# Kernel tuning notes

Hardware: AMD Instinct MI355X
Metric: run time of the kernel (lower is better)

The kernel has to match this reference:

```python
import jax, jax.numpy as jnp
import numpy as np

DIM = 1024
HEADS = 16
HEAD_DIM = DIM // HEADS
EPS = 1e-5


def layer_norm(x, w, b):
    # normalize over last dim (head_dim)
    mu = jnp.mean(x, axis=-1, keepdims=True)
    var = jnp.mean(jnp.square(x - mu), axis=-1, keepdims=True)
    return (x - mu) * jax.lax.rsqrt(var + EPS) * w + b


def setup_inputs() -> dict:
    key = jax.random.key(0)
    ks = jax.random.split(key, 8)
    B, N = 2, 2048
    x = jax.random.normal(ks[0], (B, N, DIM), dtype=jnp.float32)
    mask = jax.random.randint(ks[1], (B, 1, N, N), 0, 2) == 1  # True = masked out
    qkv_w = jax.random.normal(ks[2], (3 * DIM, DIM), dtype=jnp.float32) * (DIM ** -0.5)
    q_norm_w = jnp.ones((HEAD_DIM,), dtype=jnp.float32)
    q_norm_b = jnp.zeros((HEAD_DIM,), dtype=jnp.float32)
    k_norm_w = jnp.ones((HEAD_DIM,), dtype=jnp.float32)
    k_norm_b = jnp.zeros((HEAD_DIM,), dtype=jnp.float32)
    proj_w = jax.random.normal(ks[3], (DIM, DIM), dtype=jnp.float32) * (DIM ** -0.5)
    proj_b = jnp.zeros((DIM,), dtype=jnp.float32)
    return {"x": x, "mask": mask, "qkv_w": qkv_w,
            "q_norm_w": q_norm_w, "q_norm_b": q_norm_b,
            "k_norm_w": k_norm_w, "k_norm_b": k_norm_b,
            "proj_w": proj_w, "proj_b": proj_b}


def reference(x, mask, qkv_w, q_norm_w, q_norm_b, k_norm_w, k_norm_b, proj_w, proj_b):
    B, N, C = x.shape
    H, D = HEADS, HEAD_DIM
    scale = D ** -0.5
    # qkv projection (no bias), split into q,k,v of shape (B,H,N,D)
    qkv = (x @ qkv_w.T).reshape(B, N, 3, H, D).transpose(2, 0, 3, 1, 4)
    q, k, v = qkv[0], qkv[1], qkv[2]
    q = layer_norm(q, q_norm_w, q_norm_b)
    k = layer_norm(k, k_norm_w, k_norm_b)
    q = q * scale
    attn = jnp.einsum("bhnd,bhmd->bhnm", q, k)  # (B,H,N,N)
    attn = jnp.where(mask, -jnp.inf, attn)
    attn = jax.nn.softmax(attn, axis=-1)
    out = jnp.einsum("bhnm,bhmd->bhnd", attn, v)
    out = out.transpose(0, 2, 1, 3).reshape(B, N, C)
    return out @ proj_w.T + proj_b
```

## Files before the change

### kernel.cpp

```cpp
#include <hip/hip_runtime.h>
#include <hip/hip_bf16.h>
#include <math.h>

#define B_    2
#define N_    2048
#define DIM_  1024
#define H_    16
#define HD_   64
#define EPS_  1e-5f
#define SCALE_ 0.125f
#define LOG2E_ 1.4426950408889634f
#define MFIX_  14.0f

typedef __attribute__((ext_vector_type(8))) __bf16 bf16x8;
typedef __attribute__((ext_vector_type(8))) unsigned short ushort8;
typedef __attribute__((ext_vector_type(4))) float f32x4;
typedef __attribute__((ext_vector_type(4))) unsigned int uint4v;

__device__ __forceinline__ unsigned short f2bf(float x) {
    unsigned u = __builtin_bit_cast(unsigned, x);
    u += 0x7fff + ((u >> 16) & 1);
    return (unsigned short)(u >> 16);
}
__device__ __forceinline__ unsigned pk2bf(float a, float b) {
    unsigned ua = __builtin_bit_cast(unsigned, a) + 0x8000u;
    unsigned ub = __builtin_bit_cast(unsigned, b) + 0x8000u;
    return __builtin_amdgcn_perm(ub, ua, 0x07060302);
}

__device__ __forceinline__ void gl_lds16(const void* g, void* l) {
    __builtin_amdgcn_global_load_lds(
        (const __attribute__((address_space(1))) void*)g,
        (__attribute__((address_space(3))) void*)l, 16, 0, 0);
}

__global__ __launch_bounds__(256) void cast_all_bf16(
    const float* __restrict__ x, const float* __restrict__ qkvw,
    const float* __restrict__ pw, unsigned short* __restrict__ out) {
    int i = (blockIdx.x * 256 + threadIdx.x) * 8;
    const float* src;
    if (i < 4194304) src = x + i;
    else if (i < 7340032) src = qkvw + (i - 4194304);
    else src = pw + (i - 7340032);
    float4 v0 = *(const float4*)src;
    float4 v1 = *(const float4*)(src + 4);
    ushort8 r;
    r[0] = f2bf(v0.x); r[1] = f2bf(v0.y); r[2] = f2bf(v0.z); r[3] = f2bf(v0.w);
    r[4] = f2bf(v1.x); r[5] = f2bf(v1.y); r[6] = f2bf(v1.z); r[7] = f2bf(v1.w);
    *(ushort8*)(out + i) = r;
}

__global__ __launch_bounds__(256) void pack_mask(
    const int* __restrict__ mask, unsigned long long* __restrict__ bm) {
    int w = blockIdx.x * 4 + (threadIdx.x >> 6);
    int lane = threadIdx.x & 63;
    int mv = mask[(size_t)w * 64 + lane];
    unsigned long long bits = __ballot(mv != 0);
    if (lane == 0) bm[w] = bits;
}

__global__ __launch_bounds__(256) void gemm_qkv_ln(
    const unsigned short* __restrict__ A, const unsigned short* __restrict__ Bw,
    const float* __restrict__ qnw, const float* __restrict__ qnb,
    const float* __restrict__ knw, const float* __restrict__ knb,
    unsigned short* __restrict__ qbuf, unsigned short* __restrict__ kbuf,
    unsigned short* __restrict__ vbuf) {
    const int K = DIM_;
    __shared__ unsigned short As[128 * 32];
    __shared__ unsigned short Bs[128 * 32];
    const int tid = threadIdx.x;
    const int wave = tid >> 6, lane = tid & 63;
    const int quad = lane >> 4, lcol = lane & 15;
    const int wr = wave >> 1, wc = wave & 1;
    const int row0 = blockIdx.y * 128, col0 = blockIdx.x * 128;

    f32x4 acc[4][4];
#pragma unroll
    for (int i = 0; i < 4; ++i)
#pragma unroll
        for (int j = 0; j < 4; ++j) acc[i][j] = (f32x4){0.f, 0.f, 0.f, 0.f};

    for (int k0 = 0; k0 < K; k0 += 32) {
        __syncthreads();
#pragma unroll
        for (int c = 0; c < 2; ++c) {
            int base = wave * 2048 + c * 1024;
            int myofs = base + lane * 16;
            int r = myofs >> 6;
            int kb = myofs & 63;
            gl_lds16((const char*)A + ((size_t)(row0 + r) * K + k0) * 2 + kb,
                     (char*)As + base);
            gl_lds16((const char*)Bw + ((size_t)(col0 + r) * K + k0) * 2 + kb,
                     (char*)Bs + base);
        }
        __syncthreads();

        bf16x8 af[4], bfr[4];
#pragma unroll
        for (int i = 0; i < 4; ++i) {
            af[i] = *(const bf16x8*)&As[(wr * 64 + i * 16 + lcol) * 32 + quad * 8];
            bfr[i] = *(const bf16x8*)&Bs[(wc * 64 + i * 16 + lcol) * 32 + quad * 8];
        }
#pragma unroll
        for (int i = 0; i < 4; ++i)
#pragma unroll
            for (int j = 0; j < 4; ++j)
                acc[i][j] = __builtin_amdgcn_mfma_f32_16x16x32_bf16(
                    af[i], bfr[j], acc[i][j], 0, 0, 0);
    }

    const int colbase = col0 + wc * 64;
    const int t = colbase >> 10;
    const int h = (colbase & 1023) >> 6;

    if (t < 2) {
        const float* wv = (t == 0) ? qnw : knw;
        const float* bv = (t == 0) ? qnb : knb;
        float wreg[4], breg[4];
#pragma unroll
        for (int j = 0; j < 4; ++j) {
            wreg[j] = wv[j * 16 + lcol];
            breg[j] = bv[j * 16 + lcol];
        }
        const float sc = (t == 0) ? (SCALE_ * LOG2E_) : 1.f;
        unsigned short* obase = (t == 0) ? qbuf : kbuf;
#pragma unroll
        for (int i = 0; i < 4; ++i) {
#pragma unroll
            for (int reg = 0; reg < 4; ++reg) {
                int row = row0 + wr * 64 + i * 16 + quad * 4 + reg;
                int bb = row >> 11, n = row & (N_ - 1);
                float v[4];
#pragma unroll
                for (int j = 0; j < 4; ++j) v[j] = acc[i][j][reg];
                float s = v[0] + v[1] + v[2] + v[3];
                s += __shfl_xor(s, 1);
                s += __shfl_xor(s, 2);
                s += __shfl_xor(s, 4);
                s += __shfl_xor(s, 8);
                float mu = s * (1.f / 64.f);
                float d[4], s2 = 0.f;
#pragma unroll
                for (int j = 0; j < 4; ++j) {
                    d[j] = v[j] - mu;
                    s2 += d[j] * d[j];
                }
                s2 += __shfl_xor(s2, 1);
                s2 += __shfl_xor(s2, 2);
                s2 += __shfl_xor(s2, 4);
                s2 += __shfl_xor(s2, 8);
                float r = rsqrtf(s2 * (1.f / 64.f) + EPS_);
                float o0 = (d[0] * r * wreg[0] + breg[0]) * sc;
                float o1 = (d[1] * r * wreg[1] + breg[1]) * sc;
                float o2 = (d[2] * r * wreg[2] + breg[2]) * sc;
                float o3 = (d[3] * r * wreg[3] + breg[3]) * sc;
                uint2 pk;
                pk.x = pk2bf(o0, o1);
                pk.y = pk2bf(o2, o3);
                *(uint2*)(obase + ((size_t)(bb * H_ + h) * N_ + n) * 64 +
                          lcol * 4) = pk;
            }
        }
    } else {
#pragma unroll
        for (int i = 0; i < 4; ++i) {
#pragma unroll
            for (int reg = 0; reg < 4; ++reg) {
                int row = row0 + wr * 64 + i * 16 + quad * 4 + reg;
                uint2 pk;
                pk.x = pk2bf(acc[i][0][reg], acc[i][1][reg]);
                pk.y = pk2bf(acc[i][2][reg], acc[i][3][reg]);
                *(uint2*)(vbuf + (size_t)row * DIM_ + h * 64 + lcol * 4) = pk;
            }
        }
    }
}

__global__ __launch_bounds__(256) void gemm_proj(
    const unsigned short* __restrict__ A, const unsigned short* __restrict__ Bw,
    const float* __restrict__ bias, float* __restrict__ Cout) {
    const int K = DIM_;
    __shared__ unsigned short As[128 * 32];
    __shared__ unsigned short Bs[64 * 32];
    const int tid = threadIdx.x;
    const int wave = tid >> 6, lane = tid & 63;
    const int quad = lane >> 4, lcol = lane & 15;
    const int row0 = blockIdx.y * 128, col0 = blockIdx.x * 64;

    f32x4 acc[2][4];
#pragma unroll
    for (int i = 0; i < 2; ++i)
#pragma unroll
        for (int j = 0; j < 4; ++j) acc[i][j] = (f32x4){0.f, 0.f, 0.f, 0.f};

    for (int k0 = 0; k0 < K; k0 += 32) {
        __syncthreads();
#pragma unroll
        for (int pi = 0; pi < 3; ++pi) {
            int p = wave * 3 + pi;
            if (p < 8) {
                int base = p * 1024;
                int myofs = base + lane * 16;
                int r = myofs >> 6, kb = myofs & 63;
                gl_lds16((const char*)A + ((size_t)(row0 + r) * K + k0) * 2 + kb,
                         (char*)As + base);
            } else {
                int base = (p - 8) * 1024;
                int myofs = base + lane * 16;
                int r = myofs >> 6, kb = myofs & 63;
                gl_lds16((const char*)Bw + ((size_t)(col0 + r) * K + k0) * 2 + kb,
                         (char*)Bs + base);
            }
        }
        __syncthreads();

        bf16x8 af[2], bfr[4];
#pragma unroll
        for (int i = 0; i < 2; ++i)
            af[i] = *(const bf16x8*)&As[(wave * 32 + i * 16 + lcol) * 32 + quad * 8];
#pragma unroll
        for (int j = 0; j < 4; ++j)
            bfr[j] = *(const bf16x8*)&Bs[(j * 16 + lcol) * 32 + quad * 8];
#pragma unroll
        for (int i = 0; i < 2; ++i)
#pragma unroll
            for (int j = 0; j < 4; ++j)
                acc[i][j] = __builtin_amdgcn_mfma_f32_16x16x32_bf16(
                    af[i], bfr[j], acc[i][j], 0, 0, 0);
    }

#pragma unroll
    for (int i = 0; i < 2; ++i) {
#pragma unroll
        for (int j = 0; j < 4; ++j) {
            int col = col0 + j * 16 + lcol;
            float bv = bias[col];
#pragma unroll
            for (int reg = 0; reg < 4; ++reg) {
                int row = row0 + wave * 32 + i * 16 + quad * 4 + reg;
                Cout[(size_t)row * DIM_ + col] = acc[i][j][reg] + bv;
            }
        }
    }
}

__global__ __launch_bounds__(256) void transpose_v(
    const unsigned short* __restrict__ vbuf, unsigned short* __restrict__ vt) {
    __shared__ unsigned short Ts[64 * 65];
    const int tid = threadIdx.x;
    const int bh = blockIdx.y, n0 = blockIdx.x * 64;
    const int b = bh >> 4, h = bh & 15;
    {
        int r = tid >> 2, s = tid & 3;
        const unsigned short* src =
            vbuf + (size_t)(b * N_ + n0 + r) * DIM_ + h * 64 + s * 16;
#pragma unroll
        for (int i = 0; i < 16; ++i) {
            int p = s * 16 + i;
            int trued = (p >> 2) + (p & 3) * 16;
            Ts[r * 65 + trued] = src[i];
        }
    }
    __syncthreads();
    {
        int d = tid >> 2, kt = tid & 3;
        unsigned short* dstrow = vt + (size_t)(bh * 64 + d) * N_ + n0;
        int P = kt >> 1, t = kt & 1;
#pragma unroll
        for (int q = 0; q < 4; ++q) {
            __align__(8) unsigned short tmp4[4];
#pragma unroll
            for (int j = 0; j < 4; ++j)
                tmp4[j] = Ts[(kt * 16 + q * 4 + j) * 65 + d];
            *(uint2*)(dstrow + P * 32 + q * 8 + t * 4) = *(const uint2*)tmp4;
        }
    }
}

#define WAITBAR(Ncnt)                                                     \
    asm volatile("s_waitcnt vmcnt(" #Ncnt ")" ::: "memory");              \
    __builtin_amdgcn_s_barrier();                                         \
    __builtin_amdgcn_sched_barrier(0);

#define ISSUE(NF, PS)                                                     \
    {                                                                     \
        const int nf_ = (NF);                                             \
        gl_lds16(kgbase + ((size_t)nf_ << 13) + klo0,                     \
                 (char*)Ks[PS] + kld0);                                   \
        gl_lds16(kgbase + ((size_t)nf_ << 13) + klo1,                     \
                 (char*)Ks[PS] + kld1);                                   \
        gl_lds16(vtbase + (size_t)nf_ * 128 + vlo0,                       \
                 (char*)Vts[PS] + kld0);                                  \
        gl_lds16(vtbase + (size_t)nf_ * 128 + vlo1,                       \
                 (char*)Vts[PS] + kld1);                                  \
        mm0[PS] = bmq0[nf_];                                              \
        mm1[PS] = bmq1[nf_];                                              \
    }

#define COMPUTE(J)                                                        \
    {                                                                     \
        const unsigned long long mwa = mm0[J], mwb = mm1[J];              \
        const char* ksb = (const char*)Ks[J];                             \
        const char* vsb = (const char*)Vts[J];                            \
        f32x4 sacc[2][4];                                                 \
        {                                                                 \
            unsigned long long mqa = mwa >> (quad * 4);                   \
            unsigned long long mqb = mwb >> (quad * 4);                   \
            unsigned ml[2][2];                                            \
            ml[0][0] = (unsigned)mqa; ml[0][1] = (unsigned)(mqa >> 32);   \
            ml[1][0] = (unsigned)mqb; ml[1][1] = (unsigned)(mqb >> 32);   \
            _Pragma("unroll")                                             \
            for (int qf = 0; qf < 2; ++qf) {                              \
                _Pragma("unroll")                                         \
                for (int kt = 0; kt < 4; ++kt) {                          \
                    unsigned word = ml[qf][kt >> 1];                      \
                    const int sh = (kt & 1) * 16;                         \
                    _Pragma("unroll")                                     \
                    for (int reg = 0; reg < 4; ++reg)                     \
                        sacc[qf][kt][reg] =                               \
                            ((word >> (sh + reg)) & 1u) ? -1e4f : -MFIX_; \
                }                                                         \
            }                                                             \
        }                                                                 \
        _Pragma("unroll")                                                 \
        for (int kt = 0; kt < 4; ++kt) {                                  \
            _Pragma("unroll")                                             \
            for (int d0 = 0; d0 < 2; ++d0) {                              \
                int p = d0 * 4 + quad;                                    \
                bf16x8 ak = *(const bf16x8*)(ksb + p * 1024 +             \
                    (((kt * 16 + lcol) ^ (quad * 2)) << 4));              \
                sacc[0][kt] = __builtin_amdgcn_mfma_f32_16x16x32_bf16(    \
                    ak, bq[0][d0], sacc[0][kt], 0, 0, 0);                 \
                sacc[1][kt] = __builtin_amdgcn_mfma_f32_16x16x32_bf16(    \
                    ak, bq[1][d0], sacc[1][kt], 0, 0, 0);                 \
            }                                                             \
        }                                                                 \
        uint2 pk[2][4];                                                   \
        _Pragma("unroll")                                                 \
        for (int qf = 0; qf < 2; ++qf) {                                  \
            _Pragma("unroll")                                             \
            for (int kt = 0; kt < 4; ++kt) {                              \
                float p0 = exp2f(sacc[qf][kt][0]);                        \
                float p1 = exp2f(sacc[qf][kt][1]);                        \
                float p2 = exp2f(sacc[qf][kt][2]);                        \
                float p3 = exp2f(sacc[qf][kt][3]);                        \
                pk[qf][kt].x = pk2bf(p0, p1);                             \
                pk[qf][kt].y = pk2bf(p2, p3);                             \
            }                                                             \
        }                                                                 \
        _Pragma("unroll")                                                 \
        for (int P = 0; P < 2; ++P) {                                     \
            bf16x8 bp[2];                                                 \
            _Pragma("unroll")                                             \
            for (int qf = 0; qf < 2; ++qf) {                              \
                uint4v bu;                                                \
                bu[0] = pk[qf][2 * P].x;                                  \
                bu[1] = pk[qf][2 * P].y;                                  \
                bu[2] = pk[qf][2 * P + 1].x;                              \
                bu[3] = pk[qf][2 * P + 1].y;                              \
                bp[qf] = __builtin_bit_cast(bf16x8, bu);                  \
                lacc[qf] = __builtin_amdgcn_mfma_f32_16x16x32_bf16(       \
                    ones, bp[qf], lacc[qf], 0, 0, 0);                     \
            }                                                             \
            _Pragma("unroll")                                             \
            for (int dt = 0; dt < 4; ++dt) {                              \
                int c = P * 4 + quad;                                     \
                bf16x8 va = *(const bf16x8*)(vsb + c * 1024 +             \
                    (((dt * 16 + lcol) ^ (quad * 2)) << 4));              \
                oacc[0][dt] = __builtin_amdgcn_mfma_f32_16x16x32_bf16(    \
                    va, bp[0], oacc[0][dt], 0, 0, 0);                     \
                oacc[1][dt] = __builtin_amdgcn_mfma_f32_16x16x32_bf16(    \
                    va, bp[1], oacc[1][dt], 0, 0, 0);                     \
            }                                                             \
        }                                                                 \
    }

__global__ __launch_bounds__(256, 2) void flash_attn_mfma8(
    const unsigned short* __restrict__ q, const unsigned short* __restrict__ k,
    const unsigned short* __restrict__ vt,
    const unsigned long long* __restrict__ bm, unsigned short* __restrict__ ao) {
    __shared__ unsigned short Qs[128 * 64];
    __shared__ unsigned short Ks[4][64 * 64];
    __shared__ unsigned short Vts[4][64 * 64];

    const int tid = threadIdx.x;
    const int wave = tid >> 6, lane = tid & 63;
    const int quad = lane >> 4, lcol = lane & 15;
    const int bh = blockIdx.y, b = bh >> 4, h = bh & 15;
    const int q0 = blockIdx.x * 128;

    const char* kgbase = (const char*)k + (size_t)bh * N_ * 128;
    const char* vtbase = (const char*)vt + (size_t)bh * 64 * N_ * 2;

    const int c0 = wave * 2, c1 = wave * 2 + 1;
    const int swz0 = (c0 & 3) * 2, swz1 = (c1 & 3) * 2;
    const int klo0 = (lane ^ swz0) * 128 + c0 * 16;
    const int klo1 = (lane ^ swz1) * 128 + c1 * 16;
    const size_t vlo0 = (size_t)(lane ^ swz0) * (N_ * 2) + c0 * 16;
    const size_t vlo1 = (size_t)(lane ^ swz1) * (N_ * 2) + c1 * 16;
    const int kld0 = c0 * 1024, kld1 = c1 * 1024;

    const unsigned long long* bmq0 =
        bm + ((size_t)b * N_ + q0 + wave * 32 + lcol) * 32;
    const unsigned long long* bmq1 = bmq0 + 16 * 32;

    unsigned long long mm0[4], mm1[4];

    {
        const char* qg = (const char*)(q + (size_t)(bh * N_ + q0) * 64);
#pragma unroll
        for (int c = 0; c < 4; ++c) {
            int base = wave * 4096 + c * 1024;
            gl_lds16(qg + base + lane * 16, (char*)Qs + base);
        }
    }
    asm volatile("" ::: "memory");
    __builtin_amdgcn_sched_barrier(0);
#pragma unroll
    for (int t = 0; t < 3; ++t) {
        gl_lds16(kgbase + ((size_t)t << 13) + klo0, (char*)Ks[t] + kld0);
        gl_lds16(kgbase + ((size_t)t << 13) + klo1, (char*)Ks[t] + kld1);
        gl_lds16(vtbase + (size_t)t * 128 + vlo0, (char*)Vts[t] + kld0);
        gl_lds16(vtbase + (size_t)t * 128 + vlo1, (char*)Vts[t] + kld1);
        mm0[t] = bmq0[t];
        mm1[t] = bmq1[t];
    }
    asm volatile("s_waitcnt vmcnt(18)" ::: "memory");
    __builtin_amdgcn_sched_barrier(0);

    bf16x8 bq[2][2];
#pragma unroll
    for (int qf = 0; qf < 2; ++qf)
#pragma unroll
        for (int d0 = 0; d0 < 2; ++d0)
            bq[qf][d0] = *(const bf16x8*)&Qs[(wave * 32 + qf * 16 + lcol) * 64 +
                                             d0 * 32 + quad * 8];

    ushort8 ot;
#pragma unroll
    for (int i = 0; i < 8; ++i) ot[i] = 0x3F80;
    const bf16x8 ones = __builtin_bit_cast(bf16x8, ot);

    f32x4 oacc[2][4];
#pragma unroll
    for (int qf = 0; qf < 2; ++qf)
#pragma unroll
        for (int dt = 0; dt < 4; ++dt) oacc[qf][dt] = (f32x4){0.f, 0.f, 0.f, 0.f};
    f32x4 lacc[2];
    lacc[0] = (f32x4){0.f, 0.f, 0.f, 0.f};
    lacc[1] = (f32x4){0.f, 0.f, 0.f, 0.f};

    for (int g = 0; g < 7; ++g) {
        WAITBAR(12) ISSUE(g * 4 + 3, 3) COMPUTE(0)
        WAITBAR(12) ISSUE(g * 4 + 4, 0) COMPUTE(1)
        WAITBAR(12) ISSUE(g * 4 + 5, 1) COMPUTE(2)
        WAITBAR(12) ISSUE(g * 4 + 6, 2) COMPUTE(3)
    }
    WAITBAR(12) ISSUE(31, 3) COMPUTE(0)
    WAITBAR(12) COMPUTE(1)
    WAITBAR(6)  COMPUTE(2)
    WAITBAR(0)  COMPUTE(3)

#pragma unroll
    for (int qf = 0; qf < 2; ++qf) {
        float inv = 1.f / lacc[qf][0];
        int row = q0 + wave * 32 + qf * 16 + lcol;
        unsigned short* dst =
            ao + ((size_t)(b * N_ + row)) * DIM_ + h * 64 + quad * 4;
#pragma unroll
        for (int dt = 0; dt < 4; ++dt) {
            uint2 pko;
            pko.x = pk2bf(oacc[qf][dt][0] * inv, oacc[qf][dt][1] * inv);
            pko.y = pk2bf(oacc[qf][dt][2] * inv, oacc[qf][dt][3] * inv);
            *(uint2*)(dst + dt * 16) = pko;
        }
    }
}

extern "C" void kernel_launch(void* const* d_in, const int* in_sizes, int n_in,
                              void* d_out, int out_size, void* d_ws,
                              size_t ws_size, hipStream_t stream) {
    const float* x     = (const float*)d_in[0];
    const int*   mask  = (const int*)d_in[1];
    const float* qkv_w = (const float*)d_in[2];
    const float* qnw   = (const float*)d_in[3];
    const float* qnb   = (const float*)d_in[4];
    const float* knw   = (const float*)d_in[5];
    const float* knb   = (const float*)d_in[6];
    const float* pw    = (const float*)d_in[7];
    const float* pb    = (const float*)d_in[8];
    float* out = (float*)d_out;

    char* ws = (char*)d_ws;
    unsigned short* x_bf  = (unsigned short*)(ws + 0);
    unsigned short* qw_bf = (unsigned short*)(ws + 8388608);
    unsigned short* pw_bf = (unsigned short*)(ws + 14680064);
    unsigned short* qbuf  = (unsigned short*)(ws + 16777216);
    unsigned short* kbuf  = (unsigned short*)(ws + 25165824);
    unsigned short* vbuf  = (unsigned short*)(ws + 33554432);
    unsigned short* vt    = (unsigned short*)(ws + 41943040);
    unsigned long long* bmask = (unsigned long long*)(ws + 50331648);
    unsigned short* ao_bnc = vbuf;

    cast_all_bf16<<<8388608 / 2048, 256, 0, stream>>>(x, qkv_w, pw, x_bf);

    gemm_qkv_ln<<<dim3(3072 / 128, 4096 / 128), 256, 0, stream>>>(
        x_bf, qw_bf, qnw, qnb, knw, knb, qbuf, kbuf, vbuf);

    transpose_v<<<dim3(N_ / 64, B_ * H_), 256, 0, stream>>>(vbuf, vt);

    pack_mask<<<(B_ * N_ * (N_ / 64)) / 4, 256, 0, stream>>>(mask, bmask);

    flash_attn_mfma8<<<dim3(N_ / 128, B_ * H_), 256, 0, stream>>>(
        qbuf, kbuf, vt, bmask, ao_bnc);

    gemm_proj<<<dim3(DIM_ / 64, 4096 / 128), 256, 0, stream>>>(
        ao_bnc, pw_bf, pb, out);
}
```

Baseline: 276.0 us.

## Interleave QK^T and PV of paired KV tiles in flash attention pipeline

Restructures the flash-attention main loop so two KV tiles are processed as a pair. The QK^T of the second tile and the PV of the first are interleaved so softmax exp work overlaps MFMA. Loads are now issued two tiles at a time with full vmcnt(0) waits, and pointers are incremented instead of recomputed. It also adds s_setprio around MFMA blocks, branchless mask-to-bias selection, and a native v_cvt_pk_bf16_f32 for packing. The cost is higher register pressure from two live score tiles and coarser load/compute overlap, since each stage now waits for all outstanding loads.

```diff
diff --git a/kernel.cpp b/kernel.cpp
--- a/kernel.cpp
+++ b/kernel.cpp
@@ -26,6 +26,11 @@
     unsigned ua = __builtin_bit_cast(unsigned, a) + 0x8000u;
     unsigned ub = __builtin_bit_cast(unsigned, b) + 0x8000u;
     return __builtin_amdgcn_perm(ub, ua, 0x07060302);
+}
+__device__ __forceinline__ unsigned cvtpk(float a, float b) {
+    unsigned r;
+    asm("v_cvt_pk_bf16_f32 %0, %1, %2" : "=v"(r) : "v"(a), "v"(b));
+    return r;
 }
 
 __device__ __forceinline__ void gl_lds16(const void* g, void* l) {
@@ -282,100 +287,111 @@
     __builtin_amdgcn_s_barrier();                                         \
     __builtin_amdgcn_sched_barrier(0);
 
-#define ISSUE(NF, PS)                                                     \
+#define ISSUE2(B0, B1)                                                    \
     {                                                                     \
-        const int nf_ = (NF);                                             \
-        gl_lds16(kgbase + ((size_t)nf_ << 13) + klo0,                     \
-                 (char*)Ks[PS] + kld0);                                   \
-        gl_lds16(kgbase + ((size_t)nf_ << 13) + klo1,                     \
-                 (char*)Ks[PS] + kld1);                                   \
-        gl_lds16(vtbase + (size_t)nf_ * 128 + vlo0,                       \
-                 (char*)Vts[PS] + kld0);                                  \
-        gl_lds16(vtbase + (size_t)nf_ * 128 + vlo1,                       \
-                 (char*)Vts[PS] + kld1);                                  \
-        mm0[PS] = bmq0[nf_];                                              \
-        mm1[PS] = bmq1[nf_];                                              \
-    }
-
-#define COMPUTE(J)                                                        \
+        gl_lds16(kp0, (char*)Ks[B0] + kld0);                              \
+        gl_lds16(kp1, (char*)Ks[B0] + kld1);                              \
+        gl_lds16(vp0, (char*)Vts[B0] + kld0);                             \
+        gl_lds16(vp1, (char*)Vts[B0] + kld1);                             \
+        gl_lds16(kp0 + 8192, (char*)Ks[B1] + kld0);                       \
+        gl_lds16(kp1 + 8192, (char*)Ks[B1] + kld1);                       \
+        gl_lds16(vp0 + 128, (char*)Vts[B1] + kld0);                       \
+        gl_lds16(vp1 + 128, (char*)Vts[B1] + kld1);                       \
+        mm0[B0] = bmq0[0]; mm1[B0] = bmq1[0];                             \
+        mm0[B1] = bmq0[1]; mm1[B1] = bmq1[1];                             \
+        kp0 += 16384; kp1 += 16384; vp0 += 256; vp1 += 256;               \
+        bmq0 += 2; bmq1 += 2;                                             \
+    }
+
+#define QKT(J, SACC, MWA, MWB)                                            \
     {                                                                     \
-        const unsigned long long mwa = mm0[J], mwb = mm1[J];              \
-        const char* ksb = (const char*)Ks[J];                             \
-        const char* vsb = (const char*)Vts[J];                            \
-        f32x4 sacc[2][4];                                                 \
-        {                                                                 \
-            unsigned long long mqa = mwa >> (quad * 4);                   \
-            unsigned long long mqb = mwb >> (quad * 4);                   \
-            unsigned ml[2][2];                                            \
-            ml[0][0] = (unsigned)mqa; ml[0][1] = (unsigned)(mqa >> 32);   \
-            ml[1][0] = (unsigned)mqb; ml[1][1] = (unsigned)(mqb >> 32);   \
+        unsigned long long mqa = (MWA) >> (quad * 4);                     \
+        unsigned long long mqb = (MWB) >> (quad * 4);                     \
+        unsigned ml[2][2];                                                \
+        ml[0][0] = (unsigned)mqa; ml[0][1] = (unsigned)(mqa >> 32);       \
+        ml[1][0] = (unsigned)mqb; ml[1][1] = (unsigned)(mqb >> 32);       \
+        _Pragma("unroll")                                                 \
+        for (int qf = 0; qf < 2; ++qf)                                    \
             _Pragma("unroll")                                             \
-            for (int qf = 0; qf < 2; ++qf) {                              \
+            for (int kt = 0; kt < 4; ++kt) {                              \
+                unsigned word = ml[qf][kt >> 1];                          \
                 _Pragma("unroll")                                         \
-                for (int kt = 0; kt < 4; ++kt) {                          \
-                    unsigned word = ml[qf][kt >> 1];                      \
-                    const int sh = (kt & 1) * 16;                         \
-                    _Pragma("unroll")                                     \
-                    for (int reg = 0; reg < 4; ++reg)                     \
-                        sacc[qf][kt][reg] =                               \
-                            ((word >> (sh + reg)) & 1u) ? -1e4f : -MFIX_; \
+                for (int reg = 0; reg < 4; ++reg) {                       \
+                    unsigned msk = (unsigned)(((int)(word <<              \
+                        (31 - ((kt & 1) * 16 + reg)))) >> 31);            \
+                    SACC[qf][kt][reg] = __builtin_bit_cast(float,         \
+                        (msk & 0xc61c4000u) | (~msk & 0xc1600000u));      \
                 }                                                         \
             }                                                             \
-        }                                                                 \
+        __builtin_amdgcn_s_setprio(1);                                    \
+        _Pragma("unroll")                                                 \
+        for (int kt = 0; kt < 4; ++kt)                                    \
+            _Pragma("unroll")                                             \
+            for (int d0 = 0; d0 < 2; ++d0) {                              \
+                bf16x8 ak = *(const bf16x8*)((const char*)Ks[J] +         \
+                    (d0 * 4 + quad) * 1024 + kt * 256 + lofs);            \
+                SACC[0][kt] = __builtin_amdgcn_mfma_f32_16x16x32_bf16(    \
+                    ak, bq[0][d0], SACC[0][kt], 0, 0, 0);                 \
+                SACC[1][kt] = __builtin_amdgcn_mfma_f32_16x16x32_bf16(    \
+                    ak, bq[1][d0], SACC[1][kt], 0, 0, 0);                 \
+            }                                                             \
+        __builtin_amdgcn_s_setprio(0);                                    \
+    }
+
+#define SM(SACC, PK)                                                      \
+    _Pragma("unroll")                                                     \
+    for (int qf = 0; qf < 2; ++qf)                                        \
         _Pragma("unroll")                                                 \
         for (int kt = 0; kt < 4; ++kt) {                                  \
-            _Pragma("unroll")                                             \
-            for (int d0 = 0; d0 < 2; ++d0) {                              \
-                int p = d0 * 4 + quad;                                    \
-                bf16x8 ak = *(const bf16x8*)(ksb + p * 1024 +             \
-                    (((kt * 16 + lcol) ^ (quad * 2)) << 4));              \
-                sacc[0][kt] = __builtin_amdgcn_mfma_f32_16x16x32_bf16(    \
-                    ak, bq[0][d0], sacc[0][kt], 0, 0, 0);                 \
-                sacc[1][kt] = __builtin_amdgcn_mfma_f32_16x16x32_bf16(    \
-                    ak, bq[1][d0], sacc[1][kt], 0, 0, 0);                 \
-            }                                                             \
-        }                                                                 \
-        uint2 pk[2][4];                                                   \
-        _Pragma("unroll")                                                 \
-        for (int qf = 0; qf < 2; ++qf) {                                  \
-            _Pragma("unroll")                                             \
-            for (int kt = 0; kt < 4; ++kt) {                              \
-                float p0 = exp2f(sacc[qf][kt][0]);                        \
-                float p1 = exp2f(sacc[qf][kt][1]);                        \
-                float p2 = exp2f(sacc[qf][kt][2]);                        \
-                float p3 = exp2f(sacc[qf][kt][3]);                        \
-                pk[qf][kt].x = pk2bf(p0, p1);                             \
-                pk[qf][kt].y = pk2bf(p2, p3);                             \
-            }                                                             \
-        }                                                                 \
+            float p0 = exp2f(SACC[qf][kt][0]);                            \
+            float p1 = exp2f(SACC[qf][kt][1]);                            \
+            float p2 = exp2f(SACC[qf][kt][2]);                            \
+            float p3 = exp2f(SACC[qf][kt][3]);                            \
+            PK[qf][kt].x = cvtpk(p0, p1);                                 \
+            PK[qf][kt].y = cvtpk(p2, p3);                                 \
+        }
+
+#define PV(J, PK)                                                         \
+    {                                                                     \
+        __builtin_amdgcn_s_setprio(1);                                    \
         _Pragma("unroll")                                                 \
         for (int P = 0; P < 2; ++P) {                                     \
             bf16x8 bp[2];                                                 \
             _Pragma("unroll")                                             \
             for (int qf = 0; qf < 2; ++qf) {                              \
                 uint4v bu;                                                \
-                bu[0] = pk[qf][2 * P].x;                                  \
-                bu[1] = pk[qf][2 * P].y;                                  \
-                bu[2] = pk[qf][2 * P + 1].x;                              \
-                bu[3] = pk[qf][2 * P + 1].y;                              \
+                bu[0] = PK[qf][2 * P].x;  bu[1] = PK[qf][2 * P].y;        \
+                bu[2] = PK[qf][2 * P + 1].x; bu[3] = PK[qf][2 * P + 1].y; \
                 bp[qf] = __builtin_bit_cast(bf16x8, bu);                  \
                 lacc[qf] = __builtin_amdgcn_mfma_f32_16x16x32_bf16(       \
                     ones, bp[qf], lacc[qf], 0, 0, 0);                     \
             }                                                             \
             _Pragma("unroll")                                             \
             for (int dt = 0; dt < 4; ++dt) {                              \
-                int c = P * 4 + quad;                                     \
-                bf16x8 va = *(const bf16x8*)(vsb + c * 1024 +             \
-                    (((dt * 16 + lcol) ^ (quad * 2)) << 4));              \
+                bf16x8 va = *(const bf16x8*)((const char*)Vts[J] +        \
+                    (P * 4 + quad) * 1024 + dt * 256 + lofs);             \
                 oacc[0][dt] = __builtin_amdgcn_mfma_f32_16x16x32_bf16(    \
                     va, bp[0], oacc[0][dt], 0, 0, 0);                     \
                 oacc[1][dt] = __builtin_amdgcn_mfma_f32_16x16x32_bf16(    \
                     va, bp[1], oacc[1][dt], 0, 0, 0);                     \
             }                                                             \
         }                                                                 \
-    }
-
-__global__ __launch_bounds__(256, 2) void flash_attn_mfma8(
+        __builtin_amdgcn_s_setprio(0);                                    \
+    }
+
+#define PAIR(J0, J1)                                                      \
+    {                                                                     \
+        f32x4 saccA[2][4], saccB[2][4];                                   \
+        uint2 pkA[2][4], pkB[2][4];                                       \
+        QKT(J0, saccA, mm0[J0], mm1[J0])                                  \
+        SM(saccA, pkA)                                                    \
+        QKT(J1, saccB, mm0[J1], mm1[J1])                                  \
+        PV(J0, pkA)                                                       \
+        SM(saccB, pkB)                                                    \
+        PV(J1, pkB)                                                       \
+    }
+
+__global__ __launch_bounds__(256, 2) void flash_attn_mfma9(
     const unsigned short* __restrict__ q, const unsigned short* __restrict__ k,
     const unsigned short* __restrict__ vt,
     const unsigned long long* __restrict__ bm, unsigned short* __restrict__ ao) {
@@ -388,22 +404,22 @@
     const int quad = lane >> 4, lcol = lane & 15;
     const int bh = blockIdx.y, b = bh >> 4, h = bh & 15;
     const int q0 = blockIdx.x * 128;
+    const int lofs = (lcol ^ (quad * 2)) << 4;
 
     const char* kgbase = (const char*)k + (size_t)bh * N_ * 128;
     const char* vtbase = (const char*)vt + (size_t)bh * 64 * N_ * 2;
 
-    const int c0 = wave * 2, c1 = wave * 2 + 1;
+    const int c0 = wave * 2, c1 = c0 + 1;
     const int swz0 = (c0 & 3) * 2, swz1 = (c1 & 3) * 2;
-    const int klo0 = (lane ^ swz0) * 128 + c0 * 16;
-    const int klo1 = (lane ^ swz1) * 128 + c1 * 16;
-    const size_t vlo0 = (size_t)(lane ^ swz0) * (N_ * 2) + c0 * 16;
-    const size_t vlo1 = (size_t)(lane ^ swz1) * (N_ * 2) + c1 * 16;
     const int kld0 = c0 * 1024, kld1 = c1 * 1024;
+    const char* kp0 = kgbase + (lane ^ swz0) * 128 + c0 * 16;
+    const char* kp1 = kgbase + (lane ^ swz1) * 128 + c1 * 16;
+    const char* vp0 = vtbase + (size_t)(lane ^ swz0) * (N_ * 2) + c0 * 16;
+    const char* vp1 = vtbase + (size_t)(lane ^ swz1) * (N_ * 2) + c1 * 16;
 
     const unsigned long long* bmq0 =
         bm + ((size_t)b * N_ + q0 + wave * 32 + lcol) * 32;
     const unsigned long long* bmq1 = bmq0 + 16 * 32;
-
     unsigned long long mm0[4], mm1[4];
 
     {
@@ -417,15 +433,18 @@
     asm volatile("" ::: "memory");
     __builtin_amdgcn_sched_barrier(0);
 #pragma unroll
-    for (int t = 0; t < 3; ++t) {
-        gl_lds16(kgbase + ((size_t)t << 13) + klo0, (char*)Ks[t] + kld0);
-        gl_lds16(kgbase + ((size_t)t << 13) + klo1, (char*)Ks[t] + kld1);
-        gl_lds16(vtbase + (size_t)t * 128 + vlo0, (char*)Vts[t] + kld0);
-        gl_lds16(vtbase + (size_t)t * 128 + vlo1, (char*)Vts[t] + kld1);
+    for (int t = 0; t < 4; ++t) {
+        gl_lds16(kp0, (char*)Ks[t] + kld0);
+        gl_lds16(kp1, (char*)Ks[t] + kld1);
+        gl_lds16(vp0, (char*)Vts[t] + kld0);
+        gl_lds16(vp1, (char*)Vts[t] + kld1);
         mm0[t] = bmq0[t];
         mm1[t] = bmq1[t];
-    }
-    asm volatile("s_waitcnt vmcnt(18)" ::: "memory");
+        kp0 += 8192; kp1 += 8192; vp0 += 128; vp1 += 128;
+        __builtin_amdgcn_sched_barrier(0);
+    }
+    bmq0 += 4; bmq1 += 4;
+    asm volatile("s_waitcnt vmcnt(24)" ::: "memory");
     __builtin_amdgcn_sched_barrier(0);
 
     bf16x8 bq[2][2];
@@ -450,16 +469,18 @@
     lacc[0] = (f32x4){0.f, 0.f, 0.f, 0.f};
     lacc[1] = (f32x4){0.f, 0.f, 0.f, 0.f};
 
+    WAITBAR(12)
+    PAIR(0, 1)
     for (int g = 0; g < 7; ++g) {
-        WAITBAR(12) ISSUE(g * 4 + 3, 3) COMPUTE(0)
-        WAITBAR(12) ISSUE(g * 4 + 4, 0) COMPUTE(1)
-        WAITBAR(12) ISSUE(g * 4 + 5, 1) COMPUTE(2)
-        WAITBAR(12) ISSUE(g * 4 + 6, 2) COMPUTE(3)
-    }
-    WAITBAR(12) ISSUE(31, 3) COMPUTE(0)
-    WAITBAR(12) COMPUTE(1)
-    WAITBAR(6)  COMPUTE(2)
-    WAITBAR(0)  COMPUTE(3)
+        WAITBAR(0)
+        ISSUE2(0, 1)
+        PAIR(2, 3)
+        WAITBAR(0)
+        ISSUE2(2, 3)
+        PAIR(0, 1)
+    }
+    WAITBAR(0)
+    PAIR(2, 3)
 
 #pragma unroll
     for (int qf = 0; qf < 2; ++qf) {
@@ -511,7 +532,7 @@
 
     pack_mask<<<(B_ * N_ * (N_ / 64)) / 4, 256, 0, stream>>>(mask, bmask);
 
-    flash_attn_mfma8<<<dim3(N_ / 128, B_ * H_), 256, 0, stream>>>(
+    flash_attn_mfma9<<<dim3(N_ / 128, B_ * H_), 256, 0, stream>>>(
         qbuf, kbuf, vt, bmask, ao_bnc);
 
     gemm_proj<<<dim3(DIM_ / 64, 4096 / 128), 256, 0, stream>>>(
```

Result: no change. 273.5 us (-0.9%).
